# Optimization experiments

Hardware: AMD Instinct MI355X
Metric: run time of the kernel (lower is better)

## Reference

```python
import jax, jax.numpy as jnp
import numpy as np

L = 3          # num_layer
E_DIM = 64     # emb_dim
B = 4          # graphs per batch
N = 20000      # nodes per graph
E = 320000     # edges per graph
IN_DIM = 21    # raw node feature dim (Linear(21, emb_dim))
BN_EPS = 1e-5


def setup_inputs() -> dict:
    key = jax.random.key(0)
    ks = jax.random.split(key, 16)
    h2 = 2 * E_DIM
    inp = {
        "x": jax.random.normal(ks[0], (B, N, IN_DIM), dtype=jnp.float32),
        "edge_index": jax.random.randint(ks[1], (B, 2, E), 0, N, dtype=jnp.int64),
        "edge_attr": jax.random.normal(ks[2], (B, E, 1), dtype=jnp.float32),
        # layer-0 input node embedding Linear(21, emb)
        "inW": jax.random.normal(ks[3], (IN_DIM, E_DIM), dtype=jnp.float32) * 0.1,
        "inb": jnp.zeros((E_DIM,), dtype=jnp.float32),
        # per-layer edge encoder Linear(1, emb)
        "edgeW": jax.random.normal(ks[4], (L, 1, E_DIM), dtype=jnp.float32) * 0.1,
        "edgeb": jnp.zeros((L, E_DIM), dtype=jnp.float32),
        # per-layer MLP: Linear(2e,2e) -> BN(2e) -> ReLU -> Linear(2e,e)
        "W1": jax.random.normal(ks[5], (L, h2, h2), dtype=jnp.float32) * 0.05,
        "b1": jnp.zeros((L, h2), dtype=jnp.float32),
        "gamma": jnp.ones((L, h2), dtype=jnp.float32),
        "beta": jnp.zeros((L, h2), dtype=jnp.float32),
        "W2": jax.random.normal(ks[6], (L, h2, E_DIM), dtype=jnp.float32) * 0.05,
        "b2": jnp.zeros((L, E_DIM), dtype=jnp.float32),
    }
    return inp


def _batchnorm_train(h, g, b):
    # BatchNorm1d in training mode: per-graph stats over the node dim, biased var
    m = h.mean(axis=0)
    v = jnp.mean((h - m) ** 2, axis=0)
    return (h - m) * jax.lax.rsqrt(v + BN_EPS) * g + b


def _gin_layer(xg, eig, eag, W1l, b1l, gl, bel, W2l, b2l):
    # xg [N,e], eig [2,E], eag [E,e]
    x_j = xg[eig[0]]                                   # gather source nodes [E,e]
    msg = jnp.concatenate([x_j, eag], axis=-1)         # [E,2e]
    aggr = jax.ops.segment_sum(msg, eig[1], num_segments=N)  # scatter-add [N,2e]
    h = aggr @ W1l + b1l
    h = _batchnorm_train(h, gl, bel)
    h = jax.nn.relu(h)
    return h @ W2l + b2l                               # [N,e]


def reference(x, edge_index, edge_attr, inW, inb, edgeW, edgeb, W1, b1, gamma, beta, W2, b2):
    h = x
    for l in range(L):
        ea = edge_attr @ edgeW[l] + edgeb[l]           # [B,E,e] edge embeddings
        if l == 0:
            h = h @ inW + inb                          # [B,N,e]
        h = jax.vmap(_gin_layer, in_axes=(0, 0, 0, None, None, None, None, None, None))(
            h, edge_index, ea, W1[l], b1[l], gamma[l], beta[l], W2[l], b2[l])
        if l < L - 1:                                  # drop_ratio=0 -> dropout is identity
            h = jax.nn.relu(h)
    return h  # JK='last'
```

## Files before the change

kernel.cpp:

```cpp
#include <hip/hip_runtime.h>
#include <hip/hip_bf16.h>
#include <hip/hip_fp16.h>

#define NB 4
#define NN 20000
#define NE 320000
#define IND 21
#define ED 64
#define H2 128
#define CAP 48
#define NRANGE 32
#define RNODES 625
#define BINCAP 160
#define SCAP 11264
#define BN_EPS 1e-5f

typedef __attribute__((ext_vector_type(8))) short bf16x8;
typedef __attribute__((ext_vector_type(4))) float f32x4;

__device__ __forceinline__ short f2bf(float f) {
    unsigned u = __float_as_uint(f);
    u += 0x7fffu + ((u >> 16) & 1u);
    return (short)(u >> 16);
}

__device__ __forceinline__ void add8(float* ac, const uint4 rv) {
    const float2 f0 = __half22float2(*(const __half2*)&rv.x);
    const float2 f1 = __half22float2(*(const __half2*)&rv.y);
    const float2 f2 = __half22float2(*(const __half2*)&rv.z);
    const float2 f3 = __half22float2(*(const __half2*)&rv.w);
    ac[0] += f0.x; ac[1] += f0.y; ac[2] += f1.x; ac[3] += f1.y;
    ac[4] += f2.x; ac[5] += f2.y; ac[6] += f3.x; ac[7] += f3.y;
}


__global__ __launch_bounds__(256) void k_compact(
    const int* __restrict__ ei, const float* __restrict__ eattr,
    uint2* __restrict__ stage, int* __restrict__ rcnt)
{
    __shared__ uint2 bins[NRANGE][BINCAP];
    __shared__ int lcnt[NRANGE];
    __shared__ int lbase[NRANGE];
    const int b = blockIdx.y;
    const int e0 = blockIdx.x * 2048;
    const int tid = threadIdx.x;
    if (tid < NRANGE) lcnt[tid] = 0;
    __syncthreads();
    const int* srcp = ei + (size_t)b * 2 * NE;
    const int* dstp = srcp + NE;
    const float* ap = eattr + (size_t)b * NE;
    #pragma unroll
    for (int it = 0; it < 8; ++it) {
        const int e = e0 + it * 256 + tid;
        if (e < NE) {
            const int dst = dstp[e];
            const int src = srcp[e];
            const float a = ap[e];
            const int r = dst / RNODES;
            const unsigned lo = ((unsigned)src & 0xffffu) | (__float_as_uint(a) & 0xffff0000u);
            const int p = atomicAdd(&lcnt[r], 1);
            if (p < BINCAP) bins[r][p] = make_uint2(lo, (unsigned)dst);
        }
    }
    __syncthreads();
    if (tid < NRANGE) lbase[tid] = atomicAdd(&rcnt[b * NRANGE + tid], min(lcnt[tid], BINCAP));
    __syncthreads();
    for (int r = 0; r < NRANGE; ++r) {
        const int c = min(lcnt[r], BINCAP);
        uint2* dstg = stage + (size_t)(b * NRANGE + r) * SCAP + lbase[r];
        for (int i = tid; i < c; i += 256) dstg[i] = bins[r][i];
    }
}

__global__ __launch_bounds__(256) void k_scatter(
    const uint2* __restrict__ stage, const int* __restrict__ rcnt,
    int* __restrict__ cnt, unsigned int* __restrict__ bucket)
{
    const int b = blockIdx.x >> 5;
    const int g = blockIdx.x & 31;
    const int count = min(rcnt[b * NRANGE + g], SCAP);
    const uint2* st = stage + (size_t)(b * NRANGE + g) * SCAP;
    for (int idx = threadIdx.x; idx < count; idx += 256) {
        const uint2 rec = st[idx];
        const int node = b * NN + (int)rec.y;
        const int p = atomicAdd(&cnt[node], 1);
        if (p < CAP) bucket[(size_t)node * CAP + p] = rec.x;
    }
}

__global__ __launch_bounds__(256) void k_in(
    const float* __restrict__ x, const float* __restrict__ inW,
    const float* __restrict__ inb, __half* __restrict__ h)
{
    const int b = blockIdx.y;
    const int t = blockIdx.x * 256 + threadIdx.x;
    const int n = t >> 6;
    const int c = t & 63;
    if (n >= NN) return;
    const float* xr = x + ((size_t)b * NN + n) * IND;
    float acc = inb[c];
    #pragma unroll
    for (int k = 0; k < IND; ++k) acc += xr[k] * inW[k * ED + c];
    h[((size_t)b * NN + n) * ED + c] = __float2half(acc);
}

__global__ __launch_bounds__(256) void k_prep(
    const float* __restrict__ W1, const float* __restrict__ W2,
    const float* __restrict__ edgeW, const float* __restrict__ edgeb,
    short* __restrict__ W1T, short* __restrict__ W2T,
    float* __restrict__ uv_all, float* __restrict__ stats_all)
{
    const int l = blockIdx.x;
    const int tid = threadIdx.x;
    ((float4*)(stats_all + l * 1024))[tid] = make_float4(0.f, 0.f, 0.f, 0.f);
    for (int i = tid; i < H2 * ED; i += 256) {
        const int j = i >> 6, k = i & 63;
        W1T[l * 8192 + i] = f2bf(W1[(size_t)l * H2 * H2 + k * H2 + j]);
    }
    for (int i = tid; i < ED * H2; i += 256) {
        const int c = i >> 7, k = i & 127;
        W2T[l * 8192 + i] = f2bf(W2[(size_t)l * H2 * ED + k * ED + c]);
    }
    if (tid < H2) {
        float u = 0.f, v = 0.f;
        for (int k = 0; k < ED; ++k) {
            const float w = W1[(size_t)l * H2 * H2 + (ED + k) * H2 + tid];
            u += edgeW[l * ED + k] * w;
            v += edgeb[l * ED + k] * w;
        }
        uv_all[l * 256 + tid] = u;
        uv_all[l * 256 + H2 + tid] = v;
    }
}


__global__ __launch_bounds__(256, 4) void k_aggr_stats(
    const __half* __restrict__ h, const unsigned int* __restrict__ bucket,
    const int* __restrict__ cnt_arr, const short* __restrict__ W1Tl,
    const float* __restrict__ b1l, const float* __restrict__ uv_l,
    __half* __restrict__ h1g, float* __restrict__ stats_l)
{
    __shared__ short atb[32 * 72];
    __shared__ float sdl[32], ddl[32];
    __shared__ float uL[H2], vL[H2], bbL[H2];
    const int tid = threadIdx.x;
    const int g = blockIdx.x & 7;
    const int b = g >> 1;
    const int t = ((int)blockIdx.x >> 3) * 2 + (g & 1);
    if (t >= NN / 32) return;
    const int n0 = t * 32;

    if (tid < H2) { uL[tid] = uv_l[tid]; vL[tid] = uv_l[H2 + tid]; bbL[tid] = b1l[tid]; }

    {
        const int node = n0 + (tid >> 3);
        const int q = tid & 7;
        const int cntraw = cnt_arr[b * NN + node];
        const int cnt = min(cntraw, CAP);
        const unsigned int* row = bucket + (size_t)(b * NN + node) * CAP;
        const __half* hp = h + (size_t)b * NN * ED + q * 8;
        float ac[8];
        #pragma unroll
        for (int i = 0; i < 8; ++i) ac[i] = 0.f;
        float sa = 0.f;
        int j = 0;
        for (; j + 8 <= cnt; j += 8) {
            const uint4 sA = *(const uint4*)(row + j);
            const uint4 sB = *(const uint4*)(row + j + 4);
            const uint4 r0 = *(const uint4*)(hp + (size_t)(sA.x & 0xffffu) * ED);
            const uint4 r1 = *(const uint4*)(hp + (size_t)(sA.y & 0xffffu) * ED);
            const uint4 r2 = *(const uint4*)(hp + (size_t)(sA.z & 0xffffu) * ED);
            const uint4 r3 = *(const uint4*)(hp + (size_t)(sA.w & 0xffffu) * ED);
            const uint4 r4 = *(const uint4*)(hp + (size_t)(sB.x & 0xffffu) * ED);
            const uint4 r5 = *(const uint4*)(hp + (size_t)(sB.y & 0xffffu) * ED);
            const uint4 r6 = *(const uint4*)(hp + (size_t)(sB.z & 0xffffu) * ED);
            const uint4 r7 = *(const uint4*)(hp + (size_t)(sB.w & 0xffffu) * ED);
            sa += __uint_as_float(sA.x & 0xffff0000u) + __uint_as_float(sA.y & 0xffff0000u)
                + __uint_as_float(sA.z & 0xffff0000u) + __uint_as_float(sA.w & 0xffff0000u)
                + __uint_as_float(sB.x & 0xffff0000u) + __uint_as_float(sB.y & 0xffff0000u)
                + __uint_as_float(sB.z & 0xffff0000u) + __uint_as_float(sB.w & 0xffff0000u);
            add8(ac, r0); add8(ac, r1); add8(ac, r2); add8(ac, r3);
            add8(ac, r4); add8(ac, r5); add8(ac, r6); add8(ac, r7);
        }
        for (; j + 4 <= cnt; j += 4) {
            const uint4 ss = *(const uint4*)(row + j);
            const uint4 r0 = *(const uint4*)(hp + (size_t)(ss.x & 0xffffu) * ED);
            const uint4 r1 = *(const uint4*)(hp + (size_t)(ss.y & 0xffffu) * ED);
            const uint4 r2 = *(const uint4*)(hp + (size_t)(ss.z & 0xffffu) * ED);
            const uint4 r3 = *(const uint4*)(hp + (size_t)(ss.w & 0xffffu) * ED);
            sa += __uint_as_float(ss.x & 0xffff0000u) + __uint_as_float(ss.y & 0xffff0000u)
                + __uint_as_float(ss.z & 0xffff0000u) + __uint_as_float(ss.w & 0xffff0000u);
            add8(ac, r0); add8(ac, r1); add8(ac, r2); add8(ac, r3);
        }
        for (; j < cnt; ++j) {
            const unsigned e = row[j];
            sa += __uint_as_float(e & 0xffff0000u);
            const uint4 r0 = *(const uint4*)(hp + (size_t)(e & 0xffffu) * ED);
            add8(ac, r0);
        }
        uint4 pk;
        pk.x = (unsigned short)f2bf(ac[0]) | ((unsigned int)(unsigned short)f2bf(ac[1]) << 16);
        pk.y = (unsigned short)f2bf(ac[2]) | ((unsigned int)(unsigned short)f2bf(ac[3]) << 16);
        pk.z = (unsigned short)f2bf(ac[4]) | ((unsigned int)(unsigned short)f2bf(ac[5]) << 16);
        pk.w = (unsigned short)f2bf(ac[6]) | ((unsigned int)(unsigned short)f2bf(ac[7]) << 16);
        *(uint4*)&atb[(tid >> 3) * 72 + q * 8] = pk;
        if (q == 0) {
            sdl[tid >> 3] = sa;
            ddl[tid >> 3] = (float)cntraw;
        }
    }
    __syncthreads();

    const int l = tid & 63;
    const int w = tid >> 6;
    const int m = l & 15, quad = l >> 4;
    const int mt = w & 1;
    const int jb = (w >> 1) * 4;
    f32x4 acc[4];
    #pragma unroll
    for (int i = 0; i < 4; ++i) acc[i] = (f32x4){0.f, 0.f, 0.f, 0.f};
    #pragma unroll
    for (int kc = 0; kc < 2; ++kc) {
        const bf16x8 fa = *(const bf16x8*)&atb[(mt * 16 + m) * 72 + kc * 32 + quad * 8];
        #pragma unroll
        for (int t2 = 0; t2 < 4; ++t2) {
            const bf16x8 fb = *(const bf16x8*)&W1Tl[((jb + t2) * 16 + m) * 64 + kc * 32 + quad * 8];
            acc[t2] = __builtin_amdgcn_mfma_f32_16x16x32_bf16(fa, fb, acc[t2], 0, 0, 0);
        }
    }
    float sa_r[4], dg_r[4];
    #pragma unroll
    for (int r = 0; r < 4; ++r) {
        const int row = mt * 16 + quad * 4 + r;
        sa_r[r] = sdl[row]; dg_r[r] = ddl[row];
    }
    #pragma unroll
    for (int t2 = 0; t2 < 4; ++t2) {
        const int j = (jb + t2) * 16 + m;
        const float u = uL[j], v = vL[j], bb = bbL[j];
        float ls = 0.f, lq = 0.f;
        #pragma unroll
        for (int r = 0; r < 4; ++r) {
            const float h1v = acc[t2][r] + sa_r[r] * u + dg_r[r] * v + bb;
            h1g[((size_t)b * NN + n0 + mt * 16 + quad * 4 + r) * H2 + j] = __float2half(h1v);
            ls += h1v; lq += h1v * h1v;
        }
        ls += __shfl_xor(ls, 16); ls += __shfl_xor(ls, 32);
        lq += __shfl_xor(lq, 16); lq += __shfl_xor(lq, 32);
        if (l < 16) {
            atomicAdd(&stats_l[b * H2 + j], ls);
            atomicAdd(&stats_l[NB * H2 + b * H2 + j], lq);
        }
    }
}

__global__ __launch_bounds__(256) void k_mlp_out(
    const __half* __restrict__ h1g, const short* __restrict__ W2Tl,
    const float* __restrict__ stats_l, const float* __restrict__ gamma_l,
    const float* __restrict__ beta_l, const float* __restrict__ b2l,
    __half* __restrict__ outh, float* __restrict__ outf, int last)
{
    __shared__ short wt[ED * 136];
    __shared__ short pb[64 * 136];
    const int tid = threadIdx.x;
    const int g = blockIdx.x & 7;
    const int b = g >> 1;
    const int t = ((int)blockIdx.x >> 3) * 2 + (g & 1);
    if (t >= (NN + 63) / 64) return;
    const int n0 = t * 64;

    const uint4* h1p = (const uint4*)(h1g + ((size_t)b * NN + n0) * H2);
    const uint4 hv0 = h1p[tid];
    const uint4 hv1 = h1p[tid + 256];
    const uint4 hv2 = h1p[tid + 512];
    const uint4 hv3 = h1p[tid + 768];

    for (int i = tid; i < 1024; i += 256)
        *(uint4*)&wt[(i >> 4) * 136 + (i & 15) * 8] = ((const uint4*)W2Tl)[i];

    const int ch0 = (tid & 15) * 8;
    float sc[8], sh[8];
    #pragma unroll
    for (int e = 0; e < 8; ++e) {
        const int j = ch0 + e;
        const float mm = stats_l[b * H2 + j] * (1.f / NN);
        const float var = fmaxf(stats_l[NB * H2 + b * H2 + j] * (1.f / NN) - mm * mm, 0.f);
        const float rs = rsqrtf(var + BN_EPS);
        sc[e] = gamma_l[j] * rs;
        sh[e] = beta_l[j] - mm * sc[e];
    }

    {
        uint4 hv;
        short ob[8];
        #define BN8(K, HV)                                                    \
        {                                                                     \
            hv = HV;                                                          \
            const __half* hp = (const __half*)&hv;                            \
            _Pragma("unroll")                                                 \
            for (int e = 0; e < 8; ++e) {                                     \
                const float xv = __half2float(hp[e]);                         \
                ob[e] = f2bf(fmaxf(xv * sc[e] + sh[e], 0.f));                 \
            }                                                                 \
            *(uint4*)&pb[((tid >> 4) + (K) * 16) * 136 + ch0] = *(uint4*)ob;  \
        }
        BN8(0, hv0) BN8(1, hv1) BN8(2, hv2) BN8(3, hv3)
        #undef BN8
    }
    __syncthreads();

    {
        const int l = tid & 63;
        const int w = tid >> 6;
        const int m = l & 15, quad = l >> 4;
        f32x4 acc2[4];
        #pragma unroll
        for (int i = 0; i < 4; ++i) acc2[i] = (f32x4){0.f, 0.f, 0.f, 0.f};
        #pragma unroll
        for (int kc = 0; kc < 4; ++kc) {
            const bf16x8 fa = *(const bf16x8*)&pb[(w * 16 + m) * 136 + kc * 32 + quad * 8];
            #pragma unroll
            for (int t2 = 0; t2 < 4; ++t2) {
                const bf16x8 fb = *(const bf16x8*)&wt[(t2 * 16 + m) * 136 + kc * 32 + quad * 8];
                acc2[t2] = __builtin_amdgcn_mfma_f32_16x16x32_bf16(fa, fb, acc2[t2], 0, 0, 0);
            }
        }
        #pragma unroll
        for (int t2 = 0; t2 < 4; ++t2) {
            const int c = t2 * 16 + m;
            const float bb2 = b2l[c];
            #pragma unroll
            for (int r = 0; r < 4; ++r) {
                const int row = w * 16 + quad * 4 + r;
                const int n = n0 + row;
                if (n < NN) {
                    const size_t idx = ((size_t)b * NN + n) * ED + c;
                    float o = acc2[t2][r] + bb2;
                    if (last) outf[idx] = o;
                    else outh[idx] = __float2half(fmaxf(o, 0.f));
                }
            }
        }
    }
}


extern "C" void kernel_launch(void* const* d_in, const int* in_sizes, int n_in,
                              void* d_out, int out_size, void* d_ws, size_t ws_size,
                              hipStream_t stream) {
    const float* x     = (const float*)d_in[0];
    const int*   ei    = (const int*)d_in[1];
    const float* eattr = (const float*)d_in[2];
    const float* inW   = (const float*)d_in[3];
    const float* inb   = (const float*)d_in[4];
    const float* edgeW = (const float*)d_in[5];
    const float* edgeb = (const float*)d_in[6];
    const float* W1    = (const float*)d_in[7];
    const float* b1    = (const float*)d_in[8];
    const float* gamma = (const float*)d_in[9];
    const float* beta  = (const float*)d_in[10];
    const float* W2    = (const float*)d_in[11];
    const float* b2    = (const float*)d_in[12];
    float* out = (float*)d_out;

    int*   cnt    = (int*)d_ws;
    int*   rcnt   = cnt + NB * NN;
    uint2* stage  = (uint2*)(rcnt + 128);
    unsigned int* bucket = (unsigned int*)(stage + (size_t)NB * NRANGE * SCAP);
    __half* hh    = (__half*)(bucket + (size_t)NB * NN * CAP);
    __half* h1g   = hh + (size_t)NB * NN * ED;
    short* W1T    = (short*)(h1g + (size_t)NB * NN * H2);
    short* W2T    = W1T + 3 * 8192;
    float* uv_all = (float*)(W2T + 3 * 8192);
    float* stats  = uv_all + 3 * 256;

    hipMemsetAsync(cnt, 0, ((size_t)NB * NN + 128) * sizeof(int), stream);

    k_compact<<<dim3((NE + 2047) / 2048, NB), 256, 0, stream>>>(ei, eattr, stage, rcnt);
    k_scatter<<<NB * NRANGE, 256, 0, stream>>>(stage, rcnt, cnt, bucket);
    k_in<<<dim3(NN * ED / 256, NB), 256, 0, stream>>>(x, inW, inb, hh);
    k_prep<<<3, 256, 0, stream>>>(W1, W2, edgeW, edgeb, W1T, W2T, uv_all, stats);

    const int nblk1 = 8 * ((NN / 32 + 1) / 2);
    const int nblk2 = 8 * (((NN + 63) / 64 + 1) / 2);
    for (int l = 0; l < 3; ++l) {
        k_aggr_stats<<<nblk1, 256, 0, stream>>>(hh, bucket, cnt,
            W1T + l * 8192, b1 + l * H2, uv_all + l * 256,
            h1g, stats + l * 1024);
        k_mlp_out<<<nblk2, 256, 0, stream>>>(h1g,
            W2T + l * 8192, stats + l * 1024,
            gamma + l * H2, beta + l * H2, b2 + l * ED,
            hh, out, (l == 2) ? 1 : 0);
    }
}
```

Baseline: 360.7 us.

## Fuse all GIN layers into one persistent cooperative kernel with grid syncs

Replaces the six per-layer launches (aggregate+stats, then BN+MLP out) with a single persistent cooperative kernel that loops over layers and phases, using grid.sync between them. The MLP-out phase now processes 32-node tiles, matching the aggregation tiling, and reuses a shared-memory union buffer. This is meant to remove kernel launch gaps and tail effects. In exchange it adds grid-wide barrier cost and caps occupancy at the number of co-resident blocks. The CU count of 256 is hardcoded.

```diff
diff --git a/kernel.cpp b/kernel.cpp
--- a/kernel.cpp
+++ b/kernel.cpp
@@ -1,6 +1,9 @@
 #include <hip/hip_runtime.h>
 #include <hip/hip_bf16.h>
 #include <hip/hip_fp16.h>
+#include <hip/hip_cooperative_groups.h>
+
+namespace cg = cooperative_groups;
 
 #define NB 4
 #define NN 20000
@@ -133,214 +136,219 @@
     }
 }
 
-
-__global__ __launch_bounds__(256, 4) void k_aggr_stats(
-    const __half* __restrict__ h, const unsigned int* __restrict__ bucket,
-    const int* __restrict__ cnt_arr, const short* __restrict__ W1Tl,
-    const float* __restrict__ b1l, const float* __restrict__ uv_l,
-    __half* __restrict__ h1g, float* __restrict__ stats_l)
+__global__ __launch_bounds__(256, 6) void k_layers(
+    __half* __restrict__ hh, const unsigned int* __restrict__ bucket,
+    const int* __restrict__ cnt_arr, const short* __restrict__ W1T,
+    const float* __restrict__ b1, const float* __restrict__ uv_all,
+    __half* __restrict__ h1g, float* __restrict__ stats,
+    const short* __restrict__ W2T, const float* __restrict__ gammaP,
+    const float* __restrict__ betaP, const float* __restrict__ b2P,
+    float* __restrict__ outf)
 {
-    __shared__ short atb[32 * 72];
-    __shared__ float sdl[32], ddl[32];
-    __shared__ float uL[H2], vL[H2], bbL[H2];
+    __shared__ __align__(16) char smem[26112];
+    short* atb = (short*)smem;
+    float* sdl = (float*)(smem + 4608);
+    float* ddl = (float*)(smem + 4736);
+    float* uL  = (float*)(smem + 4864);
+    float* vL  = (float*)(smem + 5376);
+    float* bbL = (float*)(smem + 5888);
+    short* wt  = (short*)smem;
+    short* pb  = (short*)(smem + 17408);
+
     const int tid = threadIdx.x;
-    const int g = blockIdx.x & 7;
+    const int bid = blockIdx.x;
+    const int NBLK = gridDim.x;
+    const int g = bid & 7;
     const int b = g >> 1;
-    const int t = ((int)blockIdx.x >> 3) * 2 + (g & 1);
-    if (t >= NN / 32) return;
-    const int n0 = t * 32;
-
-    if (tid < H2) { uL[tid] = uv_l[tid]; vL[tid] = uv_l[H2 + tid]; bbL[tid] = b1l[tid]; }
-
-    {
-        const int node = n0 + (tid >> 3);
-        const int q = tid & 7;
-        const int cntraw = cnt_arr[b * NN + node];
-        const int cnt = min(cntraw, CAP);
-        const unsigned int* row = bucket + (size_t)(b * NN + node) * CAP;
-        const __half* hp = h + (size_t)b * NN * ED + q * 8;
-        float ac[8];
+    const int ln = tid & 63;
+    const int w = tid >> 6;
+    const int m = ln & 15, quad = ln >> 4;
+    cg::grid_group grid = cg::this_grid();
+
+    for (int l = 0; l < 3; ++l) {
+        const short* W1Tl = W1T + l * 8192;
+        const float* uv_l = uv_all + l * 256;
+        float* stats_l = stats + l * 1024;
+        if (tid < H2) {
+            uL[tid] = uv_l[tid]; vL[tid] = uv_l[H2 + tid];
+            bbL[tid] = (b1 + l * H2)[tid];
+        }
+        for (int wk = bid; wk < 2504; wk += NBLK) {
+            const int t = ((wk >> 3) * 2) + (g & 1);
+            const bool act = (t < 625);
+            const int n0 = t * 32;
+            if (act) {
+                const int node = n0 + (tid >> 3);
+                const int q = tid & 7;
+                const int cntraw = cnt_arr[b * NN + node];
+                const int cnt = min(cntraw, CAP);
+                const unsigned int* row = bucket + (size_t)(b * NN + node) * CAP;
+                const __half* hp = hh + (size_t)b * NN * ED + q * 8;
+                float ac[8];
+                #pragma unroll
+                for (int i = 0; i < 8; ++i) ac[i] = 0.f;
+                float sa = 0.f;
+                int j = 0;
+                for (; j + 8 <= cnt; j += 8) {
+                    const uint4 sA = *(const uint4*)(row + j);
+                    const uint4 sB = *(const uint4*)(row + j + 4);
+                    const uint4 r0 = *(const uint4*)(hp + (size_t)(sA.x & 0xffffu) * ED);
+                    const uint4 r1 = *(const uint4*)(hp + (size_t)(sA.y & 0xffffu) * ED);
+                    const uint4 r2 = *(const uint4*)(hp + (size_t)(sA.z & 0xffffu) * ED);
+                    const uint4 r3 = *(const uint4*)(hp + (size_t)(sA.w & 0xffffu) * ED);
+                    const uint4 r4 = *(const uint4*)(hp + (size_t)(sB.x & 0xffffu) * ED);
+                    const uint4 r5 = *(const uint4*)(hp + (size_t)(sB.y & 0xffffu) * ED);
+                    const uint4 r6 = *(const uint4*)(hp + (size_t)(sB.z & 0xffffu) * ED);
+                    const uint4 r7 = *(const uint4*)(hp + (size_t)(sB.w & 0xffffu) * ED);
+                    sa += __uint_as_float(sA.x & 0xffff0000u) + __uint_as_float(sA.y & 0xffff0000u)
+                        + __uint_as_float(sA.z & 0xffff0000u) + __uint_as_float(sA.w & 0xffff0000u)
+                        + __uint_as_float(sB.x & 0xffff0000u) + __uint_as_float(sB.y & 0xffff0000u)
+                        + __uint_as_float(sB.z & 0xffff0000u) + __uint_as_float(sB.w & 0xffff0000u);
+                    add8(ac, r0); add8(ac, r1); add8(ac, r2); add8(ac, r3);
+                    add8(ac, r4); add8(ac, r5); add8(ac, r6); add8(ac, r7);
+                }
+                for (; j + 4 <= cnt; j += 4) {
+                    const uint4 ss = *(const uint4*)(row + j);
+                    const uint4 r0 = *(const uint4*)(hp + (size_t)(ss.x & 0xffffu) * ED);
+                    const uint4 r1 = *(const uint4*)(hp + (size_t)(ss.y & 0xffffu) * ED);
+                    const uint4 r2 = *(const uint4*)(hp + (size_t)(ss.z & 0xffffu) * ED);
+                    const uint4 r3 = *(const uint4*)(hp + (size_t)(ss.w & 0xffffu) * ED);
+                    sa += __uint_as_float(ss.x & 0xffff0000u) + __uint_as_float(ss.y & 0xffff0000u)
+                        + __uint_as_float(ss.z & 0xffff0000u) + __uint_as_float(ss.w & 0xffff0000u);
+                    add8(ac, r0); add8(ac, r1); add8(ac, r2); add8(ac, r3);
+                }
+                for (; j < cnt; ++j) {
+                    const unsigned e = row[j];
+                    sa += __uint_as_float(e & 0xffff0000u);
+                    const uint4 r0 = *(const uint4*)(hp + (size_t)(e & 0xffffu) * ED);
+                    add8(ac, r0);
+                }
+                uint4 pk;
+                pk.x = (unsigned short)f2bf(ac[0]) | ((unsigned int)(unsigned short)f2bf(ac[1]) << 16);
+                pk.y = (unsigned short)f2bf(ac[2]) | ((unsigned int)(unsigned short)f2bf(ac[3]) << 16);
+                pk.z = (unsigned short)f2bf(ac[4]) | ((unsigned int)(unsigned short)f2bf(ac[5]) << 16);
+                pk.w = (unsigned short)f2bf(ac[6]) | ((unsigned int)(unsigned short)f2bf(ac[7]) << 16);
+                *(uint4*)&atb[(tid >> 3) * 72 + q * 8] = pk;
+                if (q == 0) {
+                    sdl[tid >> 3] = sa;
+                    ddl[tid >> 3] = (float)cntraw;
+                }
+            }
+            __syncthreads();
+            if (act) {
+                const int mt = w & 1;
+                const int jb = (w >> 1) * 4;
+                f32x4 acc[4];
+                #pragma unroll
+                for (int i = 0; i < 4; ++i) acc[i] = (f32x4){0.f, 0.f, 0.f, 0.f};
+                #pragma unroll
+                for (int kc = 0; kc < 2; ++kc) {
+                    const bf16x8 fa = *(const bf16x8*)&atb[(mt * 16 + m) * 72 + kc * 32 + quad * 8];
+                    #pragma unroll
+                    for (int t2 = 0; t2 < 4; ++t2) {
+                        const bf16x8 fb = *(const bf16x8*)&W1Tl[((jb + t2) * 16 + m) * 64 + kc * 32 + quad * 8];
+                        acc[t2] = __builtin_amdgcn_mfma_f32_16x16x32_bf16(fa, fb, acc[t2], 0, 0, 0);
+                    }
+                }
+                float sa_r[4], dg_r[4];
+                #pragma unroll
+                for (int r = 0; r < 4; ++r) {
+                    const int rrow = mt * 16 + quad * 4 + r;
+                    sa_r[r] = sdl[rrow]; dg_r[r] = ddl[rrow];
+                }
+                #pragma unroll
+                for (int t2 = 0; t2 < 4; ++t2) {
+                    const int j = (jb + t2) * 16 + m;
+                    const float u = uL[j], v = vL[j], bb = bbL[j];
+                    float ls = 0.f, lq = 0.f;
+                    #pragma unroll
+                    for (int r = 0; r < 4; ++r) {
+                        const float h1v = acc[t2][r] + sa_r[r] * u + dg_r[r] * v + bb;
+                        h1g[((size_t)b * NN + n0 + mt * 16 + quad * 4 + r) * H2 + j] = __float2half(h1v);
+                        ls += h1v; lq += h1v * h1v;
+                    }
+                    ls += __shfl_xor(ls, 16); ls += __shfl_xor(ls, 32);
+                    lq += __shfl_xor(lq, 16); lq += __shfl_xor(lq, 32);
+                    if (ln < 16) {
+                        atomicAdd(&stats_l[b * H2 + j], ls);
+                        atomicAdd(&stats_l[NB * H2 + b * H2 + j], lq);
+                    }
+                }
+            }
+            __syncthreads();
+        }
+        grid.sync();
+        const int ch0 = (tid & 15) * 8;
+        float sc[8], sh[8];
         #pragma unroll
-        for (int i = 0; i < 8; ++i) ac[i] = 0.f;
-        float sa = 0.f;
-        int j = 0;
-        for (; j + 8 <= cnt; j += 8) {
-            const uint4 sA = *(const uint4*)(row + j);
-            const uint4 sB = *(const uint4*)(row + j + 4);
-            const uint4 r0 = *(const uint4*)(hp + (size_t)(sA.x & 0xffffu) * ED);
-            const uint4 r1 = *(const uint4*)(hp + (size_t)(sA.y & 0xffffu) * ED);
-            const uint4 r2 = *(const uint4*)(hp + (size_t)(sA.z & 0xffffu) * ED);
-            const uint4 r3 = *(const uint4*)(hp + (size_t)(sA.w & 0xffffu) * ED);
-            const uint4 r4 = *(const uint4*)(hp + (size_t)(sB.x & 0xffffu) * ED);
-            const uint4 r5 = *(const uint4*)(hp + (size_t)(sB.y & 0xffffu) * ED);
-            const uint4 r6 = *(const uint4*)(hp + (size_t)(sB.z & 0xffffu) * ED);
-            const uint4 r7 = *(const uint4*)(hp + (size_t)(sB.w & 0xffffu) * ED);
-            sa += __uint_as_float(sA.x & 0xffff0000u) + __uint_as_float(sA.y & 0xffff0000u)
-                + __uint_as_float(sA.z & 0xffff0000u) + __uint_as_float(sA.w & 0xffff0000u)
-                + __uint_as_float(sB.x & 0xffff0000u) + __uint_as_float(sB.y & 0xffff0000u)
-                + __uint_as_float(sB.z & 0xffff0000u) + __uint_as_float(sB.w & 0xffff0000u);
-            add8(ac, r0); add8(ac, r1); add8(ac, r2); add8(ac, r3);
-            add8(ac, r4); add8(ac, r5); add8(ac, r6); add8(ac, r7);
-        }
-        for (; j + 4 <= cnt; j += 4) {
-            const uint4 ss = *(const uint4*)(row + j);
-            const uint4 r0 = *(const uint4*)(hp + (size_t)(ss.x & 0xffffu) * ED);
-            const uint4 r1 = *(const uint4*)(hp + (size_t)(ss.y & 0xffffu) * ED);
-            const uint4 r2 = *(const uint4*)(hp + (size_t)(ss.z & 0xffffu) * ED);
-            const uint4 r3 = *(const uint4*)(hp + (size_t)(ss.w & 0xffffu) * ED);
-            sa += __uint_as_float(ss.x & 0xffff0000u) + __uint_as_float(ss.y & 0xffff0000u)
-                + __uint_as_float(ss.z & 0xffff0000u) + __uint_as_float(ss.w & 0xffff0000u);
-            add8(ac, r0); add8(ac, r1); add8(ac, r2); add8(ac, r3);
-        }
-        for (; j < cnt; ++j) {
-            const unsigned e = row[j];
-            sa += __uint_as_float(e & 0xffff0000u);
-            const uint4 r0 = *(const uint4*)(hp + (size_t)(e & 0xffffu) * ED);
-            add8(ac, r0);
-        }
-        uint4 pk;
-        pk.x = (unsigned short)f2bf(ac[0]) | ((unsigned int)(unsigned short)f2bf(ac[1]) << 16);
-        pk.y = (unsigned short)f2bf(ac[2]) | ((unsigned int)(unsigned short)f2bf(ac[3]) << 16);
-        pk.z = (unsigned short)f2bf(ac[4]) | ((unsigned int)(unsigned short)f2bf(ac[5]) << 16);
-        pk.w = (unsigned short)f2bf(ac[6]) | ((unsigned int)(unsigned short)f2bf(ac[7]) << 16);
-        *(uint4*)&atb[(tid >> 3) * 72 + q * 8] = pk;
-        if (q == 0) {
-            sdl[tid >> 3] = sa;
-            ddl[tid >> 3] = (float)cntraw;
-        }
-    }
-    __syncthreads();
-
-    const int l = tid & 63;
-    const int w = tid >> 6;
-    const int m = l & 15, quad = l >> 4;
-    const int mt = w & 1;
-    const int jb = (w >> 1) * 4;
-    f32x4 acc[4];
-    #pragma unroll
-    for (int i = 0; i < 4; ++i) acc[i] = (f32x4){0.f, 0.f, 0.f, 0.f};
-    #pragma unroll
-    for (int kc = 0; kc < 2; ++kc) {
-        const bf16x8 fa = *(const bf16x8*)&atb[(mt * 16 + m) * 72 + kc * 32 + quad * 8];
-        #pragma unroll
-        for (int t2 = 0; t2 < 4; ++t2) {
-            const bf16x8 fb = *(const bf16x8*)&W1Tl[((jb + t2) * 16 + m) * 64 + kc * 32 + quad * 8];
-            acc[t2] = __builtin_amdgcn_mfma_f32_16x16x32_bf16(fa, fb, acc[t2], 0, 0, 0);
-        }
-    }
-    float sa_r[4], dg_r[4];
-    #pragma unroll
-    for (int r = 0; r < 4; ++r) {
-        const int row = mt * 16 + quad * 4 + r;
-        sa_r[r] = sdl[row]; dg_r[r] = ddl[row];
-    }
-    #pragma unroll
-    for (int t2 = 0; t2 < 4; ++t2) {
-        const int j = (jb + t2) * 16 + m;
-        const float u = uL[j], v = vL[j], bb = bbL[j];
-        float ls = 0.f, lq = 0.f;
-        #pragma unroll
-        for (int r = 0; r < 4; ++r) {
-            const float h1v = acc[t2][r] + sa_r[r] * u + dg_r[r] * v + bb;
-            h1g[((size_t)b * NN + n0 + mt * 16 + quad * 4 + r) * H2 + j] = __float2half(h1v);
-            ls += h1v; lq += h1v * h1v;
-        }
-        ls += __shfl_xor(ls, 16); ls += __shfl_xor(ls, 32);
-        lq += __shfl_xor(lq, 16); lq += __shfl_xor(lq, 32);
-        if (l < 16) {
-            atomicAdd(&stats_l[b * H2 + j], ls);
-            atomicAdd(&stats_l[NB * H2 + b * H2 + j], lq);
-        }
-    }
-}
-
-__global__ __launch_bounds__(256) void k_mlp_out(
-    const __half* __restrict__ h1g, const short* __restrict__ W2Tl,
-    const float* __restrict__ stats_l, const float* __restrict__ gamma_l,
-    const float* __restrict__ beta_l, const float* __restrict__ b2l,
-    __half* __restrict__ outh, float* __restrict__ outf, int last)
-{
-    __shared__ short wt[ED * 136];
-    __shared__ short pb[64 * 136];
-    const int tid = threadIdx.x;
-    const int g = blockIdx.x & 7;
-    const int b = g >> 1;
-    const int t = ((int)blockIdx.x >> 3) * 2 + (g & 1);
-    if (t >= (NN + 63) / 64) return;
-    const int n0 = t * 64;
-
-    const uint4* h1p = (const uint4*)(h1g + ((size_t)b * NN + n0) * H2);
-    const uint4 hv0 = h1p[tid];
-    const uint4 hv1 = h1p[tid + 256];
-    const uint4 hv2 = h1p[tid + 512];
-    const uint4 hv3 = h1p[tid + 768];
-
-    for (int i = tid; i < 1024; i += 256)
-        *(uint4*)&wt[(i >> 4) * 136 + (i & 15) * 8] = ((const uint4*)W2Tl)[i];
-
-    const int ch0 = (tid & 15) * 8;
-    float sc[8], sh[8];
-    #pragma unroll
-    for (int e = 0; e < 8; ++e) {
-        const int j = ch0 + e;
-        const float mm = stats_l[b * H2 + j] * (1.f / NN);
-        const float var = fmaxf(stats_l[NB * H2 + b * H2 + j] * (1.f / NN) - mm * mm, 0.f);
-        const float rs = rsqrtf(var + BN_EPS);
-        sc[e] = gamma_l[j] * rs;
-        sh[e] = beta_l[j] - mm * sc[e];
-    }
-
-    {
-        uint4 hv;
-        short ob[8];
-        #define BN8(K, HV)                                                    \
-        {                                                                     \
-            hv = HV;                                                          \
-            const __half* hp = (const __half*)&hv;                            \
-            _Pragma("unroll")                                                 \
-            for (int e = 0; e < 8; ++e) {                                     \
-                const float xv = __half2float(hp[e]);                         \
-                ob[e] = f2bf(fmaxf(xv * sc[e] + sh[e], 0.f));                 \
-            }                                                                 \
-            *(uint4*)&pb[((tid >> 4) + (K) * 16) * 136 + ch0] = *(uint4*)ob;  \
-        }
-        BN8(0, hv0) BN8(1, hv1) BN8(2, hv2) BN8(3, hv3)
-        #undef BN8
-    }
-    __syncthreads();
-
-    {
-        const int l = tid & 63;
-        const int w = tid >> 6;
-        const int m = l & 15, quad = l >> 4;
-        f32x4 acc2[4];
-        #pragma unroll
-        for (int i = 0; i < 4; ++i) acc2[i] = (f32x4){0.f, 0.f, 0.f, 0.f};
-        #pragma unroll
-        for (int kc = 0; kc < 4; ++kc) {
-            const bf16x8 fa = *(const bf16x8*)&pb[(w * 16 + m) * 136 + kc * 32 + quad * 8];
-            #pragma unroll
-            for (int t2 = 0; t2 < 4; ++t2) {
-                const bf16x8 fb = *(const bf16x8*)&wt[(t2 * 16 + m) * 136 + kc * 32 + quad * 8];
-                acc2[t2] = __builtin_amdgcn_mfma_f32_16x16x32_bf16(fa, fb, acc2[t2], 0, 0, 0);
+        for (int e = 0; e < 8; ++e) {
+            const int j = ch0 + e;
+            const float mm = stats_l[b * H2 + j] * (1.f / NN);
+            const float var = fmaxf(stats_l[NB * H2 + b * H2 + j] * (1.f / NN) - mm * mm, 0.f);
+            const float rs = rsqrtf(var + BN_EPS);
+            sc[e] = (gammaP + l * H2)[j] * rs;
+            sh[e] = (betaP + l * H2)[j] - mm * sc[e];
+        }
+        for (int i = tid; i < 1024; i += 256)
+            *(uint4*)&wt[(i >> 4) * 136 + (i & 15) * 8] = ((const uint4*)(W2T + l * 8192))[i];
+        const int last = (l == 2);
+        for (int wk = bid; wk < 2504; wk += NBLK) {
+            const int t = ((wk >> 3) * 2) + (g & 1);
+            const bool act = (t < 625);
+            const int n0 = t * 32;
+            if (act) {
+                const uint4* h1p = (const uint4*)(h1g + ((size_t)b * NN + n0) * H2);
+                const uint4 hv0 = h1p[tid];
+                const uint4 hv1 = h1p[tid + 256];
+                short ob[8];
+                {
+                    const __half* hp = (const __half*)&hv0;
+                    #pragma unroll
+                    for (int e = 0; e < 8; ++e)
+                        ob[e] = f2bf(fmaxf(__half2float(hp[e]) * sc[e] + sh[e], 0.f));
+                    *(uint4*)&pb[(tid >> 4) * 136 + ch0] = *(uint4*)ob;
+                }
+                {
+                    const __half* hp = (const __half*)&hv1;
+                    #pragma unroll
+                    for (int e = 0; e < 8; ++e)
+                        ob[e] = f2bf(fmaxf(__half2float(hp[e]) * sc[e] + sh[e], 0.f));
+                    *(uint4*)&pb[((tid >> 4) + 16) * 136 + ch0] = *(uint4*)ob;
+                }
             }
-        }
-        #pragma unroll
-        for (int t2 = 0; t2 < 4; ++t2) {
-            const int c = t2 * 16 + m;
-            const float bb2 = b2l[c];
-            #pragma unroll
-            for (int r = 0; r < 4; ++r) {
-                const int row = w * 16 + quad * 4 + r;
-                const int n = n0 + row;
-                if (n < NN) {
-                    const size_t idx = ((size_t)b * NN + n) * ED + c;
-                    float o = acc2[t2][r] + bb2;
-                    if (last) outf[idx] = o;
-                    else outh[idx] = __float2half(fmaxf(o, 0.f));
+            __syncthreads();
+            if (act) {
+                const int mt = w & 1;
+                const int ntb = (w >> 1) * 2;
+                f32x4 acc2[2];
+                acc2[0] = (f32x4){0.f, 0.f, 0.f, 0.f};
+                acc2[1] = (f32x4){0.f, 0.f, 0.f, 0.f};
+                #pragma unroll
+                for (int kc = 0; kc < 4; ++kc) {
+                    const bf16x8 fa = *(const bf16x8*)&pb[(mt * 16 + m) * 136 + kc * 32 + quad * 8];
+                    #pragma unroll
+                    for (int tt = 0; tt < 2; ++tt) {
+                        const bf16x8 fb = *(const bf16x8*)&wt[((ntb + tt) * 16 + m) * 136 + kc * 32 + quad * 8];
+                        acc2[tt] = __builtin_amdgcn_mfma_f32_16x16x32_bf16(fa, fb, acc2[tt], 0, 0, 0);
+                    }
+                }
+                #pragma unroll
+                for (int tt = 0; tt < 2; ++tt) {
+                    const int c = (ntb + tt) * 16 + m;
+                    const float bb2 = (b2P + l * ED)[c];
+                    #pragma unroll
+                    for (int r = 0; r < 4; ++r) {
+                        const int n = n0 + mt * 16 + quad * 4 + r;
+                        const size_t idx = ((size_t)b * NN + n) * ED + c;
+                        const float o = acc2[tt][r] + bb2;
+                        if (last) outf[idx] = o;
+                        else hh[idx] = __float2half(fmaxf(o, 0.f));
+                    }
                 }
             }
-        }
+            __syncthreads();
+        }
+        if (l < 2) grid.sync();
     }
 }
 
@@ -381,15 +389,19 @@
     k_in<<<dim3(NN * ED / 256, NB), 256, 0, stream>>>(x, inW, inb, hh);
     k_prep<<<3, 256, 0, stream>>>(W1, W2, edgeW, edgeb, W1T, W2T, uv_all, stats);
 
-    const int nblk1 = 8 * ((NN / 32 + 1) / 2);
-    const int nblk2 = 8 * (((NN + 63) / 64 + 1) / 2);
-    for (int l = 0; l < 3; ++l) {
-        k_aggr_stats<<<nblk1, 256, 0, stream>>>(hh, bucket, cnt,
-            W1T + l * 8192, b1 + l * H2, uv_all + l * 256,
-            h1g, stats + l * 1024);
-        k_mlp_out<<<nblk2, 256, 0, stream>>>(h1g,
-            W2T + l * 8192, stats + l * 1024,
-            gamma + l * H2, beta + l * H2, b2 + l * ED,
-            hh, out, (l == 2) ? 1 : 0);
-    }
-}
+    static int s_nblk = 0;
+    if (s_nblk == 0) {
+        int occ = 0;
+        hipOccupancyMaxActiveBlocksPerMultiprocessor(&occ, k_layers, 256, 0);
+        if (occ < 1) occ = 1;
+        int nb = occ * 256;
+        if (nb > 2504) nb = 2504;
+        s_nblk = nb;
+    }
+    void* args[] = {
+        (void*)&hh, (void*)&bucket, (void*)&cnt, (void*)&W1T, (void*)&b1,
+        (void*)&uv_all, (void*)&h1g, (void*)&stats, (void*)&W2T,
+        (void*)&gamma, (void*)&beta, (void*)&b2, (void*)&out
+    };
+    hipLaunchCooperativeKernel(k_layers, dim3(s_nblk), dim3(256), args, 0u, stream);
+}
```

After: 925.5 us. 157% more time.

## Split each node's neighbor gather across two thread groups, halve tile rows

Applied to the files above, without the earlier changes.

The aggregation kernel now handles 16 nodes per block instead of 32. Each node's edge list is split between two 8-thread halves that interleave quad-chunks, and their partial sums are merged with a shuffle. The MFMA stage is reshaped so each wave computes two 16-column tiles of a single 16-row tile. The aim is to shorten per-thread gather chains and raise memory-level parallelism and block count. The cost is more blocks, more per-block overhead (the u/v/b1 load), and twice as many stats atomics per node.

```diff
diff --git a/kernel.cpp b/kernel.cpp
--- a/kernel.cpp
+++ b/kernel.cpp
@@ -140,21 +140,22 @@
     const float* __restrict__ b1l, const float* __restrict__ uv_l,
     __half* __restrict__ h1g, float* __restrict__ stats_l)
 {
-    __shared__ short atb[32 * 72];
-    __shared__ float sdl[32], ddl[32];
+    __shared__ short atb[16 * 72];
+    __shared__ float sdl[16], ddl[16];
     __shared__ float uL[H2], vL[H2], bbL[H2];
     const int tid = threadIdx.x;
     const int g = blockIdx.x & 7;
     const int b = g >> 1;
     const int t = ((int)blockIdx.x >> 3) * 2 + (g & 1);
-    if (t >= NN / 32) return;
-    const int n0 = t * 32;
+    const int n0 = t * 16;
 
     if (tid < H2) { uL[tid] = uv_l[tid]; vL[tid] = uv_l[H2 + tid]; bbL[tid] = b1l[tid]; }
 
     {
-        const int node = n0 + (tid >> 3);
-        const int q = tid & 7;
+        const int node = n0 + (tid >> 4);
+        const int sub = tid & 15;
+        const int q = sub & 7;
+        const int par = sub >> 3;
         const int cntraw = cnt_arr[b * NN + node];
         const int cnt = min(cntraw, CAP);
         const unsigned int* row = bucket + (size_t)(b * NN + node) * CAP;
@@ -163,10 +164,11 @@
         #pragma unroll
         for (int i = 0; i < 8; ++i) ac[i] = 0.f;
         float sa = 0.f;
-        int j = 0;
-        for (; j + 8 <= cnt; j += 8) {
-            const uint4 sA = *(const uint4*)(row + j);
-            const uint4 sB = *(const uint4*)(row + j + 4);
+        const int nq = cnt >> 2;
+        int qq = par;
+        for (; qq + 2 < nq; qq += 4) {
+            const uint4 sA = *(const uint4*)(row + qq * 4);
+            const uint4 sB = *(const uint4*)(row + (qq + 2) * 4);
             const uint4 r0 = *(const uint4*)(hp + (size_t)(sA.x & 0xffffu) * ED);
             const uint4 r1 = *(const uint4*)(hp + (size_t)(sA.y & 0xffffu) * ED);
             const uint4 r2 = *(const uint4*)(hp + (size_t)(sA.z & 0xffffu) * ED);
@@ -182,31 +184,38 @@
             add8(ac, r0); add8(ac, r1); add8(ac, r2); add8(ac, r3);
             add8(ac, r4); add8(ac, r5); add8(ac, r6); add8(ac, r7);
         }
-        for (; j + 4 <= cnt; j += 4) {
-            const uint4 ss = *(const uint4*)(row + j);
-            const uint4 r0 = *(const uint4*)(hp + (size_t)(ss.x & 0xffffu) * ED);
-            const uint4 r1 = *(const uint4*)(hp + (size_t)(ss.y & 0xffffu) * ED);
-            const uint4 r2 = *(const uint4*)(hp + (size_t)(ss.z & 0xffffu) * ED);
-            const uint4 r3 = *(const uint4*)(hp + (size_t)(ss.w & 0xffffu) * ED);
-            sa += __uint_as_float(ss.x & 0xffff0000u) + __uint_as_float(ss.y & 0xffff0000u)
-                + __uint_as_float(ss.z & 0xffff0000u) + __uint_as_float(ss.w & 0xffff0000u);
+        for (; qq < nq; qq += 2) {
+            const uint4 sA = *(const uint4*)(row + qq * 4);
+            const uint4 r0 = *(const uint4*)(hp + (size_t)(sA.x & 0xffffu) * ED);
+            const uint4 r1 = *(const uint4*)(hp + (size_t)(sA.y & 0xffffu) * ED);
+            const uint4 r2 = *(const uint4*)(hp + (size_t)(sA.z & 0xffffu) * ED);
+            const uint4 r3 = *(const uint4*)(hp + (size_t)(sA.w & 0xffffu) * ED);
+            sa += __uint_as_float(sA.x & 0xffff0000u) + __uint_as_float(sA.y & 0xffff0000u)
+                + __uint_as_float(sA.z & 0xffff0000u) + __uint_as_float(sA.w & 0xffff0000u);
             add8(ac, r0); add8(ac, r1); add8(ac, r2); add8(ac, r3);
         }
-        for (; j < cnt; ++j) {
-            const unsigned e = row[j];
-            sa += __uint_as_float(e & 0xffff0000u);
-            const uint4 r0 = *(const uint4*)(hp + (size_t)(e & 0xffffu) * ED);
-            add8(ac, r0);
-        }
-        uint4 pk;
-        pk.x = (unsigned short)f2bf(ac[0]) | ((unsigned int)(unsigned short)f2bf(ac[1]) << 16);
-        pk.y = (unsigned short)f2bf(ac[2]) | ((unsigned int)(unsigned short)f2bf(ac[3]) << 16);
-        pk.z = (unsigned short)f2bf(ac[4]) | ((unsigned int)(unsigned short)f2bf(ac[5]) << 16);
-        pk.w = (unsigned short)f2bf(ac[6]) | ((unsigned int)(unsigned short)f2bf(ac[7]) << 16);
-        *(uint4*)&atb[(tid >> 3) * 72 + q * 8] = pk;
-        if (q == 0) {
-            sdl[tid >> 3] = sa;
-            ddl[tid >> 3] = (float)cntraw;
+        if ((nq & 1) == par) {
+            for (int p = nq * 4; p < cnt; ++p) {
+                const unsigned e = row[p];
+                sa += __uint_as_float(e & 0xffff0000u);
+                const uint4 r0 = *(const uint4*)(hp + (size_t)(e & 0xffffu) * ED);
+                add8(ac, r0);
+            }
+        }
+        #pragma unroll
+        for (int i = 0; i < 8; ++i) ac[i] += __shfl_xor(ac[i], 8);
+        sa += __shfl_xor(sa, 8);
+        if (par == 0) {
+            uint4 pk;
+            pk.x = (unsigned short)f2bf(ac[0]) | ((unsigned int)(unsigned short)f2bf(ac[1]) << 16);
+            pk.y = (unsigned short)f2bf(ac[2]) | ((unsigned int)(unsigned short)f2bf(ac[3]) << 16);
+            pk.z = (unsigned short)f2bf(ac[4]) | ((unsigned int)(unsigned short)f2bf(ac[5]) << 16);
+            pk.w = (unsigned short)f2bf(ac[6]) | ((unsigned int)(unsigned short)f2bf(ac[7]) << 16);
+            *(uint4*)&atb[(tid >> 4) * 72 + q * 8] = pk;
+            if (q == 0) {
+                sdl[tid >> 4] = sa;
+                ddl[tid >> 4] = (float)cntraw;
+            }
         }
     }
     __syncthreads();
@@ -214,16 +223,15 @@
     const int l = tid & 63;
     const int w = tid >> 6;
     const int m = l & 15, quad = l >> 4;
-    const int mt = w & 1;
-    const int jb = (w >> 1) * 4;
-    f32x4 acc[4];
-    #pragma unroll
-    for (int i = 0; i < 4; ++i) acc[i] = (f32x4){0.f, 0.f, 0.f, 0.f};
+    const int jb = w * 2;
+    f32x4 acc[2];
+    acc[0] = (f32x4){0.f, 0.f, 0.f, 0.f};
+    acc[1] = (f32x4){0.f, 0.f, 0.f, 0.f};
     #pragma unroll
     for (int kc = 0; kc < 2; ++kc) {
-        const bf16x8 fa = *(const bf16x8*)&atb[(mt * 16 + m) * 72 + kc * 32 + quad * 8];
-        #pragma unroll
-        for (int t2 = 0; t2 < 4; ++t2) {
+        const bf16x8 fa = *(const bf16x8*)&atb[m * 72 + kc * 32 + quad * 8];
+        #pragma unroll
+        for (int t2 = 0; t2 < 2; ++t2) {
             const bf16x8 fb = *(const bf16x8*)&W1Tl[((jb + t2) * 16 + m) * 64 + kc * 32 + quad * 8];
             acc[t2] = __builtin_amdgcn_mfma_f32_16x16x32_bf16(fa, fb, acc[t2], 0, 0, 0);
         }
@@ -231,18 +239,18 @@
     float sa_r[4], dg_r[4];
     #pragma unroll
     for (int r = 0; r < 4; ++r) {
-        const int row = mt * 16 + quad * 4 + r;
+        const int row = quad * 4 + r;
         sa_r[r] = sdl[row]; dg_r[r] = ddl[row];
     }
     #pragma unroll
-    for (int t2 = 0; t2 < 4; ++t2) {
+    for (int t2 = 0; t2 < 2; ++t2) {
         const int j = (jb + t2) * 16 + m;
         const float u = uL[j], v = vL[j], bb = bbL[j];
         float ls = 0.f, lq = 0.f;
         #pragma unroll
         for (int r = 0; r < 4; ++r) {
             const float h1v = acc[t2][r] + sa_r[r] * u + dg_r[r] * v + bb;
-            h1g[((size_t)b * NN + n0 + mt * 16 + quad * 4 + r) * H2 + j] = __float2half(h1v);
+            h1g[((size_t)b * NN + n0 + quad * 4 + r) * H2 + j] = __float2half(h1v);
             ls += h1v; lq += h1v * h1v;
         }
         ls += __shfl_xor(ls, 16); ls += __shfl_xor(ls, 32);
@@ -381,7 +389,7 @@
     k_in<<<dim3(NN * ED / 256, NB), 256, 0, stream>>>(x, inW, inb, hh);
     k_prep<<<3, 256, 0, stream>>>(W1, W2, edgeW, edgeb, W1T, W2T, uv_all, stats);
 
-    const int nblk1 = 8 * ((NN / 32 + 1) / 2);
+    const int nblk1 = 8 * 625;
     const int nblk2 = 8 * (((NN + 63) / 64 + 1) / 2);
     for (int l = 0; l < 3; ++l) {
         k_aggr_stats<<<nblk1, 256, 0, stream>>>(hh, bucket, cnt,
```

New measurement: 357.6 us. Within noise of the previous version (-0.9%).
